# Optimization experiments

Measured on AMD Instinct MI355X. Metric: run time of the kernel, lower is better.

## Reference

```python
import jax, jax.numpy as jnp
import numpy as np

B, H, W = 4, 192, 448
BWEIGHT = 5.0   # backward_weight for level 3
K, P, DC = 5, 2, 25  # unfold/dist kernel, padding, dist channels


def conv(x, w, b, pad):
    y = jax.lax.conv_general_dilated(x, w, (1, 1), pad,
                                     dimension_numbers=('NCHW', 'OIHW', 'NCHW'))
    return y + b[None, :, None, None]


def lrelu(x):
    return jnp.where(x >= 0, x, 0.1 * x)


def backwarp(img, flow):
    # bilinear backward warp, zero padding, align_corners=True convention
    _, C, h, w = img.shape
    yy, xx = jnp.meshgrid(jnp.arange(h, dtype=img.dtype), jnp.arange(w, dtype=img.dtype), indexing='ij')
    x = xx[None] + flow[:, 0]  # [B,H,W] absolute sample coords
    y = yy[None] + flow[:, 1]
    x0 = jnp.floor(x); y0 = jnp.floor(y)
    wx1 = x - x0; wy1 = y - y0
    wx0 = 1.0 - wx1; wy0 = 1.0 - wy1

    def gather(yi, xi):
        valid = ((yi >= 0) & (yi < h) & (xi >= 0) & (xi < w)).astype(img.dtype)
        yc = jnp.clip(yi, 0, h - 1).astype(jnp.int32)
        xc = jnp.clip(xi, 0, w - 1).astype(jnp.int32)
        v = jax.vmap(lambda im, yv, xv: im[:, yv, xv])(img, yc, xc)  # [B,C,H,W]
        return v * valid[:, None]

    return (gather(y0, x0) * (wy0 * wx0)[:, None] + gather(y0, x0 + 1) * (wy0 * wx1)[:, None]
            + gather(y0 + 1, x0) * (wy1 * wx0)[:, None] + gather(y0 + 1, x0 + 1) * (wy1 * wx1)[:, None])


def unfold1(x):
    # x: [B,1,H,W] -> [B,K*K,H,W], patch order (kh,kw) row-major like torch unfold
    return jax.lax.conv_general_dilated_patches(x, (K, K), (1, 1), ((P, P), (P, P)))


def setup_inputs() -> dict:
    key = jax.random.key(0)
    ks = jax.random.split(key, 24)
    f32 = jnp.float32
    inp = {
        'tensor1': jax.random.normal(ks[0], (B, 3, H, W), f32),
        'tensor2': jax.random.normal(ks[1], (B, 3, H, W), f32),
        'features_tensor1': jax.random.normal(ks[2], (B, 64, H, W), f32),
        'features_tensor2': jax.random.normal(ks[3], (B, 64, H, W), f32),
        'flow_tensor': jax.random.normal(ks[4], (B, 2, H, W), f32) * 2.0,
    }

    def wgt(i, shape):
        fan = int(np.prod(shape[1:]))
        return jax.random.normal(ks[i], shape, f32) / np.sqrt(fan)

    inp['feat_w'] = wgt(5, (128, 64, 1, 1)); inp['feat_b'] = jnp.zeros((128,), f32)
    inp['main_w1'] = wgt(6, (128, 131, 3, 3)); inp['main_b1'] = jnp.zeros((128,), f32)
    inp['main_w2'] = wgt(7, (128, 128, 3, 3)); inp['main_b2'] = jnp.zeros((128,), f32)
    inp['main_w3'] = wgt(8, (64, 128, 3, 3)); inp['main_b3'] = jnp.zeros((64,), f32)
    inp['main_w4'] = wgt(9, (64, 64, 3, 3)); inp['main_b4'] = jnp.zeros((64,), f32)
    inp['main_w5'] = wgt(10, (32, 64, 3, 3)); inp['main_b5'] = jnp.zeros((32,), f32)
    inp['main_w6'] = wgt(11, (32, 32, 3, 3)); inp['main_b6'] = jnp.zeros((32,), f32)
    inp['dist_w1'] = wgt(12, (DC, 32, K, 1)); inp['dist_b1'] = jnp.zeros((DC,), f32)
    inp['dist_w2'] = wgt(13, (DC, DC, 1, K)); inp['dist_b2'] = jnp.zeros((DC,), f32)
    inp['sx_w'] = wgt(14, (1, DC, 1, 1)); inp['sx_b'] = jnp.zeros((1,), f32)
    inp['sy_w'] = wgt(15, (1, DC, 1, 1)); inp['sy_b'] = jnp.zeros((1,), f32)
    return inp


def reference(tensor1, tensor2, features_tensor1, features_tensor2, flow_tensor,
              feat_w, feat_b, main_w1, main_b1, main_w2, main_b2, main_w3, main_b3,
              main_w4, main_b4, main_w5, main_b5, main_w6, main_b6,
              dist_w1, dist_b1, dist_w2, dist_b2, sx_w, sx_b, sy_w, sy_b):
    z = ((0, 0), (0, 0))
    o = ((1, 1), (1, 1))
    warp = backwarp(tensor2, flow_tensor * BWEIGHT)
    diff = jax.lax.stop_gradient(jnp.sqrt(jnp.sum((tensor1 - warp) ** 2, axis=1, keepdims=True)))
    feat = lrelu(conv(features_tensor1, feat_w, feat_b, z))
    flow_c = flow_tensor - jnp.mean(flow_tensor, axis=(2, 3), keepdims=True)
    x = jnp.concatenate([diff, flow_c, feat], axis=1)  # [B,131,H,W]
    for w, b in [(main_w1, main_b1), (main_w2, main_b2), (main_w3, main_b3),
                 (main_w4, main_b4), (main_w5, main_b5), (main_w6, main_b6)]:
        x = lrelu(conv(x, w, b, o))
    dist = conv(x, dist_w1, dist_b1, ((P, P), (0, 0)))   # 5x1 conv
    dist = conv(dist, dist_w2, dist_b2, ((0, 0), (P, P)))  # 1x5 conv
    dist = -(dist * dist)
    dist = jnp.exp(dist - jnp.max(dist, axis=1, keepdims=True))  # [B,25,H,W]
    divisor = 1.0 / jnp.sum(dist, axis=1, keepdims=True)
    u1 = unfold1(flow_tensor[:, 0:1])  # [B,25,H,W]
    u2 = unfold1(flow_tensor[:, 1:2])
    sx = conv(dist * u1, sx_w, sx_b, z) * divisor
    sy = conv(dist * u2, sy_w, sy_b, z) * divisor
    return jnp.concatenate([sx, sy], axis=1)
```

## Files before the change

kernel.cpp:

```cpp
#include <hip/hip_runtime.h>
#include <math.h>

#define HH 192
#define WW 448
#define HW (HH * WW)
#define PW2 450
#define PH2 194
#define NPAD 87300
#define NPADT 87552
#define GUARD 1024
#define NB 4

typedef _Float16 half8 __attribute__((ext_vector_type(8)));
typedef _Float16 half4v __attribute__((ext_vector_type(4)));
typedef float float4v __attribute__((ext_vector_type(4)));

__global__ void mean_kernel(const float* __restrict__ flow, float* __restrict__ means) {
    int bc = blockIdx.x;
    const float* src = flow + (size_t)bc * HW;
    float s = 0.f;
    for (int i = threadIdx.x; i < HW; i += 256) s += src[i];
    __shared__ float red[256];
    red[threadIdx.x] = s;
    __syncthreads();
    for (int off = 128; off > 0; off >>= 1) {
        if (threadIdx.x < off) red[threadIdx.x] += red[threadIdx.x + off];
        __syncthreads();
    }
    if (threadIdx.x == 0) means[bc] = red[0] * (1.0f / (float)HW);
}

__global__ void wtrans_kernel(const float* __restrict__ w, _Float16* __restrict__ wt,
                              int cinReal, int nchunk, int cout, int nshift, int perm,
                              int total) {
    int idx = blockIdx.x * 256 + threadIdx.x;
    if (idx >= total) return;
    int k = idx & 31;
    int r = idx >> 5;
    int m = r % cout;
    int r2 = r / cout;
    int q = r2 % nchunk;
    int s = r2 / nchunk;
    int icb = q * 32 + k;
    float val = 0.f;
    if (perm) {
        if (icb < 131) {
            int icr = (icb < 128) ? icb + 3 : icb - 128;
            val = w[((size_t)m * cinReal + icr) * nshift + s];
        }
    } else if (icb < cinReal) {
        val = w[((size_t)m * cinReal + icb) * nshift + s];
    }
    wt[idx] = (_Float16)val;
}

__global__ void feat_transpose(const float* __restrict__ feat, _Float16* __restrict__ F,
                               size_t fSlot) {
    __shared__ _Float16 tile[64 * 72];
    int t = threadIdx.x;
    int z = blockIdx.y;
    int pix0 = blockIdx.x * 64;
    const float* src = feat + (size_t)z * 64 * HW + pix0;
#pragma unroll
    for (int pass = 0; pass < 16; ++pass) {
        int c = pass * 4 + (t >> 6);
        int pl = t & 63;
        tile[pl * 72 + c] = (_Float16)src[(size_t)c * HW + pl];
    }
    __syncthreads();
    int row = pix0 / WW;
    int xcol = pix0 - row * WW;
    size_t n0 = (size_t)(row + 1) * PW2 + xcol + 1;
    _Float16* dst = F + (size_t)z * fSlot + n0 * 64;
#pragma unroll
    for (int pass = 0; pass < 2; ++pass) {
        int pl = (t >> 3) + pass * 32;
        int seg = t & 7;
        *(half8*)&dst[(size_t)pl * 64 + seg * 8] = *(const half8*)&tile[pl * 72 + seg * 8];
    }
}

__global__ void prep_kernel(const float* __restrict__ t1, const float* __restrict__ t2,
                            const float* __restrict__ flow, const float* __restrict__ means,
                            _Float16* __restrict__ bufA, size_t aSlot) {
    int n = blockIdx.x * 256 + threadIdx.x;
    if (n >= NPAD) return;
    int z = blockIdx.y;
    _Float16* dst = bufA + (size_t)z * aSlot + (size_t)n * 160 + 128;
    int y = n / PW2, x = n - PW2 * y;
    if (y < 1 || y > HH || x < 1 || x > WW) {
        dst[0] = (_Float16)0.f; dst[1] = (_Float16)0.f; dst[2] = (_Float16)0.f;
        return;
    }
    int iy = y - 1, ix = x - 1, pix = iy * WW + ix;
    const float* fb = flow + (size_t)z * 2 * HW;
    float fx = fb[pix];
    float fy = fb[HW + pix];
    float sx = (float)ix + fx * 5.0f;
    float sy = (float)iy + fy * 5.0f;
    float fx0 = floorf(sx), fy0 = floorf(sy);
    float wx1 = sx - fx0, wy1 = sy - fy0;
    float wx0 = 1.f - wx1, wy0 = 1.f - wy1;
    int ix0 = (int)fx0, iy0 = (int)fy0;
    bool y0ok = (iy0 >= 0) && (iy0 < HH);
    bool y1ok = (iy0 + 1 >= 0) && (iy0 + 1 < HH);
    bool x0ok = (ix0 >= 0) && (ix0 < WW);
    bool x1ok = (ix0 + 1 >= 0) && (ix0 + 1 < WW);
    float d2 = 0.f;
    for (int c = 0; c < 3; ++c) {
        const float* img = t2 + ((size_t)z * 3 + c) * HW;
        float v00 = (y0ok && x0ok) ? img[iy0 * WW + ix0] : 0.f;
        float v01 = (y0ok && x1ok) ? img[iy0 * WW + ix0 + 1] : 0.f;
        float v10 = (y1ok && x0ok) ? img[(iy0 + 1) * WW + ix0] : 0.f;
        float v11 = (y1ok && x1ok) ? img[(iy0 + 1) * WW + ix0 + 1] : 0.f;
        float v = v00 * (wy0 * wx0) + v01 * (wy0 * wx1) + v10 * (wy1 * wx0) + v11 * (wy1 * wx1);
        float d = t1[((size_t)z * 3 + c) * HW + pix] - v;
        d2 += d * d;
    }
    dst[0] = (_Float16)sqrtf(d2);
    dst[1] = (_Float16)(fx - means[z * 2 + 0]);
    dst[2] = (_Float16)(fy - means[z * 2 + 1]);
}

template <int BM, int KH, int KW, int CSIN, int NCHUNK, int CSOUT>
__launch_bounds__(256, 2)
__global__ void mfma_conv(const _Float16* __restrict__ in, size_t inSlot,
                          const _Float16* __restrict__ wt,
                          const float* __restrict__ bias,
                          _Float16* __restrict__ out, size_t outSlot) {
    constexpr int MT = BM / 32;
    __shared__ __align__(16) _Float16 Alds[BM * 72];
    __shared__ __align__(16) _Float16 Blds[128 * 72];
    const int t = threadIdx.x;
    const int wave = t >> 6, lane = t & 63;
    const int wm = wave >> 1, wn = wave & 1;
    const int col = lane & 15, quad = lane >> 4;
    const int n0 = blockIdx.x * 128;
    const _Float16* inImg = in + (size_t)blockIdx.z * inSlot;
    _Float16* outImg = out + (size_t)blockIdx.z * outSlot;

    float4v acc[MT][4];
#pragma unroll
    for (int i = 0; i < MT; ++i)
#pragma unroll
        for (int j = 0; j < 4; ++j) acc[i][j] = float4v{0.f, 0.f, 0.f, 0.f};

    for (int s = 0; s < KH * KW; ++s) {
        const int off = (s / KW - KH / 2) * PW2 + (s % KW - KW / 2);
        const _Float16* bsrc = inImg + (ptrdiff_t)(n0 + off) * CSIN;
        for (int q = 0; q < NCHUNK; ++q) {
            __syncthreads();
            const _Float16* asrc = wt + ((size_t)(s * NCHUNK + q)) * BM * 32;
            for (int i = t; i < BM * 4; i += 256) {
                int m = i >> 2, kp = (i & 3) * 8;
                *(half8*)&Alds[m * 72 + kp] = *(const half8*)&asrc[m * 32 + kp];
            }
            for (int i = t; i < 512; i += 256) {
                int n = i >> 2, kp = (i & 3) * 8;
                *(half8*)&Blds[n * 72 + kp] =
                    *(const half8*)&bsrc[(ptrdiff_t)n * CSIN + q * 32 + kp];
            }
            __syncthreads();
            half8 a[MT], b[4];
#pragma unroll
            for (int mt = 0; mt < MT; ++mt)
                a[mt] = *(const half8*)&Alds[(wm * MT * 16 + mt * 16 + col) * 72 + quad * 8];
#pragma unroll
            for (int nt = 0; nt < 4; ++nt)
                b[nt] = *(const half8*)&Blds[(wn * 64 + nt * 16 + col) * 72 + quad * 8];
#pragma unroll
            for (int mt = 0; mt < MT; ++mt)
#pragma unroll
                for (int nt = 0; nt < 4; ++nt)
                    acc[mt][nt] = __builtin_amdgcn_mfma_f32_16x16x32_f16(
                        a[mt], b[nt], acc[mt][nt], 0, 0, 0);
        }
    }
#pragma unroll
    for (int mt = 0; mt < MT; ++mt) {
        const int m0 = wm * MT * 16 + mt * 16 + quad * 4;
        float bv[4];
#pragma unroll
        for (int i = 0; i < 4; ++i) bv[i] = bias[m0 + i];
#pragma unroll
        for (int nt = 0; nt < 4; ++nt) {
            int n = n0 + wn * 64 + nt * 16 + col;
            int y = n / PW2, x = n - y * PW2;
            bool ok = (y >= 1) && (y <= HH) && (x >= 1) && (x <= WW) && (n < NPAD);
            half4v h;
#pragma unroll
            for (int i = 0; i < 4; ++i) {
                float v = acc[mt][nt][i] + bv[i];
                v = (v >= 0.f) ? v : 0.1f * v;
                h[i] = ok ? (_Float16)v : (_Float16)0.f;
            }
            *(half4v*)&outImg[(size_t)n * CSOUT + m0] = h;
        }
    }
}

__global__ void dist1_kernel(const _Float16* __restrict__ in, size_t inSlot,
                             const float* __restrict__ w, const float* __restrict__ bias,
                             float* __restrict__ outD, size_t outSlot) {
    __shared__ float wl[25 * 32 * 5];
    int t = threadIdx.x;
    for (int i = t; i < 4000; i += 256) wl[i] = w[i];
    __syncthreads();
    int p = blockIdx.x * 256 + t;
    int z = blockIdx.y;
    const _Float16* inI = in + (size_t)z * inSlot;
    float* out = outD + (size_t)z * outSlot;
    int y = p / WW, x = p - y * WW;
    float acc[25];
#pragma unroll
    for (int oc = 0; oc < 25; ++oc) acc[oc] = bias[oc];
    for (int kh = 0; kh < 5; ++kh) {
        int yy = y + kh - 2;
        if (yy < 0 || yy >= HH) continue;
        const _Float16* src = inI + (size_t)((yy + 1) * PW2 + x + 1) * 32;
        _Float16 vals[32];
#pragma unroll
        for (int g = 0; g < 4; ++g) *(half8*)&vals[g * 8] = *(const half8*)&src[g * 8];
#pragma unroll
        for (int ic = 0; ic < 32; ++ic) {
            float v = (float)vals[ic];
#pragma unroll
            for (int oc = 0; oc < 25; ++oc)
                acc[oc] = fmaf(v, wl[(oc * 32 + ic) * 5 + kh], acc[oc]);
        }
    }
#pragma unroll
    for (int oc = 0; oc < 25; ++oc) out[(size_t)p * 25 + oc] = acc[oc];
}

__global__ void final_kernel(const float* __restrict__ D1, size_t d1Slot,
                             const float* __restrict__ flow,
                             const float* __restrict__ dw2, const float* __restrict__ db2,
                             const float* __restrict__ sxw, const float* __restrict__ sxb,
                             const float* __restrict__ syw, const float* __restrict__ syb,
                             float* __restrict__ out) {
    __shared__ float wl[25 * 25 * 5];
    int t = threadIdx.x;
    for (int i = t; i < 3125; i += 256) wl[i] = dw2[i];
    __syncthreads();
    int p = blockIdx.x * 256 + t;
    int z = blockIdx.y;
    const float* D = D1 + (size_t)z * d1Slot;
    int y = p / WW, x = p - y * WW;
    float acc[25];
#pragma unroll
    for (int oc = 0; oc < 25; ++oc) acc[oc] = db2[oc];
    for (int kw = 0; kw < 5; ++kw) {
        int xx = x + kw - 2;
        if (xx < 0 || xx >= WW) continue;
        const float* src = D + (size_t)(y * WW + xx) * 25;
#pragma unroll
        for (int ic = 0; ic < 25; ++ic) {
            float v = src[ic];
#pragma unroll
            for (int oc = 0; oc < 25; ++oc)
                acc[oc] = fmaf(v, wl[(oc * 25 + ic) * 5 + kw], acc[oc]);
        }
    }
    float e[25];
    float m = -1e30f;
#pragma unroll
    for (int c = 0; c < 25; ++c) {
        float d = -(acc[c] * acc[c]);
        e[c] = d;
        m = fmaxf(m, d);
    }
    float s = 0.f;
#pragma unroll
    for (int c = 0; c < 25; ++c) {
        e[c] = expf(e[c] - m);
        s += e[c];
    }
    const float* f0 = flow + (size_t)z * 2 * HW;
    const float* f1 = f0 + HW;
    float ax = sxb[0], ay = syb[0];
#pragma unroll
    for (int kh = 0; kh < 5; ++kh) {
        int iy = y + kh - 2;
        bool yok = (iy >= 0) && (iy < HH);
#pragma unroll
        for (int kw = 0; kw < 5; ++kw) {
            int ix = x + kw - 2;
            int c = kh * 5 + kw;
            float u1 = 0.f, u2 = 0.f;
            if (yok && ix >= 0 && ix < WW) {
                int q = iy * WW + ix;
                u1 = f0[q];
                u2 = f1[q];
            }
            ax = fmaf(e[c] * u1, sxw[c], ax);
            ay = fmaf(e[c] * u2, syw[c], ay);
        }
    }
    float inv = 1.0f / s;
    out[(size_t)z * 2 * HW + p] = ax * inv;
    out[(size_t)z * 2 * HW + HW + p] = ay * inv;
}

extern "C" void kernel_launch(void* const* d_in, const int* in_sizes, int n_in,
                              void* d_out, int out_size, void* d_ws, size_t ws_size,
                              hipStream_t stream) {
    const float* t1      = (const float*)d_in[0];
    const float* t2      = (const float*)d_in[1];
    const float* feat_in = (const float*)d_in[2];
    const float* flow    = (const float*)d_in[4];
    const float* feat_w  = (const float*)d_in[5];
    const float* feat_b  = (const float*)d_in[6];
    const float* w1 = (const float*)d_in[7];   const float* b1 = (const float*)d_in[8];
    const float* w2 = (const float*)d_in[9];   const float* b2 = (const float*)d_in[10];
    const float* w3 = (const float*)d_in[11];  const float* b3 = (const float*)d_in[12];
    const float* w4 = (const float*)d_in[13];  const float* b4 = (const float*)d_in[14];
    const float* w5 = (const float*)d_in[15];  const float* b5 = (const float*)d_in[16];
    const float* w6 = (const float*)d_in[17];  const float* b6 = (const float*)d_in[18];
    const float* dw1 = (const float*)d_in[19]; const float* db1 = (const float*)d_in[20];
    const float* dw2 = (const float*)d_in[21]; const float* db2 = (const float*)d_in[22];
    const float* sxw = (const float*)d_in[23]; const float* sxb = (const float*)d_in[24];
    const float* syw = (const float*)d_in[25]; const float* syb = (const float*)d_in[26];
    float* out = (float*)d_out;
    char* ws = (char*)d_ws;

    const size_t OFF_FEAT = 0;
    const size_t OFF_C1 = 8192;
    const size_t OFF_C2 = 192512;
    const size_t OFF_C3 = 339968;
    const size_t OFF_C4 = 413696;
    const size_t OFF_C5 = 450560;
    const size_t OFF_C6 = 468992;
    const size_t WT_BYTES = 478208 * 2;

    _Float16* wt = (_Float16*)ws;
    float* means = (float*)(ws + WT_BYTES);
    const size_t F0 = WT_BYTES + 64;
    const size_t F_SLOT_B = (size_t)(NPADT + 2 * GUARD) * 64 * 2;
    const size_t A_SLOT_B = (size_t)(NPADT + 2 * GUARD) * 160 * 2;
    const size_t B_SLOT_B = (size_t)(NPADT + 2 * GUARD) * 128 * 2;
    const size_t C_SLOT_B = B_SLOT_B;
    const size_t PER_IMG = F_SLOT_B + A_SLOT_B + B_SLOT_B + C_SLOT_B;
    const size_t needFull = F0 + NB * PER_IMG;
    const int step = (ws_size >= needFull) ? NB : 1;

    const size_t A0 = F0 + step * F_SLOT_B;
    const size_t B0 = A0 + step * A_SLOT_B;
    const size_t C0 = B0 + step * B_SLOT_B;

    _Float16* Fd    = (_Float16*)(ws + F0) + (size_t)GUARD * 64;
    _Float16* Ad    = (_Float16*)(ws + A0) + (size_t)GUARD * 160;
    _Float16* Bd128 = (_Float16*)(ws + B0) + (size_t)GUARD * 128;
    _Float16* Bd64  = (_Float16*)(ws + B0) + (size_t)GUARD * 64;
    _Float16* Bd32  = (_Float16*)(ws + B0) + (size_t)GUARD * 32;
    _Float16* Cd128 = (_Float16*)(ws + C0) + (size_t)GUARD * 128;
    _Float16* Cd64  = (_Float16*)(ws + C0) + (size_t)GUARD * 64;
    _Float16* Cd32  = (_Float16*)(ws + C0) + (size_t)GUARD * 32;
    float* D1 = (float*)(ws + F0);

    const size_t FSL = F_SLOT_B / 2, ASL = A_SLOT_B / 2, BSL = B_SLOT_B / 2,
                 CSL = C_SLOT_B / 2, DSL = F_SLOT_B / 4;

    mean_kernel<<<8, 256, 0, stream>>>(flow, means);

    auto wlaunch = [&](const float* src, size_t dst, int cin, int nch, int cout,
                       int nsh, int perm) {
        int total = nsh * nch * cout * 32;
        wtrans_kernel<<<(total + 255) / 256, 256, 0, stream>>>(
            src, wt + dst, cin, nch, cout, nsh, perm, total);
    };
    wlaunch(feat_w, OFF_FEAT, 64, 2, 128, 1, 0);
    wlaunch(w1, OFF_C1, 131, 5, 128, 9, 1);
    wlaunch(w2, OFF_C2, 128, 4, 128, 9, 0);
    wlaunch(w3, OFF_C3, 128, 4, 64, 9, 0);
    wlaunch(w4, OFF_C4, 64, 2, 64, 9, 0);
    wlaunch(w5, OFF_C5, 64, 2, 32, 9, 0);
    wlaunch(w6, OFF_C6, 32, 1, 32, 9, 0);

    const int NT = NPADT / 128;

    for (int b0 = 0; b0 < NB; b0 += step) {
        dim3 gconv(NT, 1, step);
        feat_transpose<<<dim3(HW / 64, step), 256, 0, stream>>>(
            feat_in + (size_t)b0 * 64 * HW, Fd, FSL);
        prep_kernel<<<dim3((NPAD + 255) / 256, step), 256, 0, stream>>>(
            t1 + (size_t)b0 * 3 * HW, t2 + (size_t)b0 * 3 * HW,
            flow + (size_t)b0 * 2 * HW, means + b0 * 2, Ad, ASL);
        mfma_conv<128, 1, 1, 64, 2, 160><<<gconv, 256, 0, stream>>>(
            Fd, FSL, wt + OFF_FEAT, feat_b, Ad, ASL);
        mfma_conv<128, 3, 3, 160, 5, 128><<<gconv, 256, 0, stream>>>(
            Ad, ASL, wt + OFF_C1, b1, Bd128, BSL);
        mfma_conv<128, 3, 3, 128, 4, 128><<<gconv, 256, 0, stream>>>(
            Bd128, BSL, wt + OFF_C2, b2, Cd128, CSL);
        mfma_conv<64, 3, 3, 128, 4, 64><<<gconv, 256, 0, stream>>>(
            Cd128, CSL, wt + OFF_C3, b3, Bd64, BSL);
        mfma_conv<64, 3, 3, 64, 2, 64><<<gconv, 256, 0, stream>>>(
            Bd64, BSL, wt + OFF_C4, b4, Cd64, CSL);
        mfma_conv<32, 3, 3, 64, 2, 32><<<gconv, 256, 0, stream>>>(
            Cd64, CSL, wt + OFF_C5, b5, Bd32, BSL);
        mfma_conv<32, 3, 3, 32, 1, 32><<<gconv, 256, 0, stream>>>(
            Bd32, BSL, wt + OFF_C6, b6, Cd32, CSL);
        dist1_kernel<<<dim3(HW / 256, step), 256, 0, stream>>>(
            Cd32, CSL, dw1, db1, D1, DSL);
        final_kernel<<<dim3(HW / 256, step), 256, 0, stream>>>(
            D1, DSL, flow + (size_t)b0 * 2 * HW, dw2, db2, sxw, sxb, syw, syb,
            out + (size_t)b0 * 2 * HW);
    }
}
```

Before: 1.373 ms.

## Load MFMA fragments directly from global memory with register double-buffering

Removes the shared-memory staging of the weight and input tiles in the implicit-GEMM conv. Each lane now loads its MFMA fragments straight from global memory, prefetching the next k-step into a second register buffer while the current one is multiplied. This removes both per-step barriers and the shared-memory footprint, and raises the occupancy hint in launch bounds. In exchange, loads are now redundant across waves (each wave fetches its own A/B pieces, relying on cache), the fully unrolled loop may inflate code size, and there is more register pressure.

```diff
diff --git a/kernel.cpp b/kernel.cpp
--- a/kernel.cpp
+++ b/kernel.cpp
@@ -123,14 +123,13 @@
 }
 
 template <int BM, int KH, int KW, int CSIN, int NCHUNK, int CSOUT>
-__launch_bounds__(256, 2)
+__launch_bounds__(256, (BM > 64) ? 3 : 4)
 __global__ void mfma_conv(const _Float16* __restrict__ in, size_t inSlot,
                           const _Float16* __restrict__ wt,
                           const float* __restrict__ bias,
                           _Float16* __restrict__ out, size_t outSlot) {
     constexpr int MT = BM / 32;
-    __shared__ __align__(16) _Float16 Alds[BM * 72];
-    __shared__ __align__(16) _Float16 Blds[128 * 72];
+    constexpr int NIT = KH * KW * NCHUNK;
     const int t = threadIdx.x;
     const int wave = t >> 6, lane = t & 63;
     const int wm = wave >> 1, wn = wave & 1;
@@ -139,43 +138,42 @@
     const _Float16* inImg = in + (size_t)blockIdx.z * inSlot;
     _Float16* outImg = out + (size_t)blockIdx.z * outSlot;
 
+    const _Float16* aBase = wt + ((size_t)(wm * MT * 16 + col)) * 32 + quad * 8;
+    const _Float16* bBase = inImg + ((ptrdiff_t)(n0 + wn * 64 + col)) * CSIN + quad * 8;
+
     float4v acc[MT][4];
 #pragma unroll
     for (int i = 0; i < MT; ++i)
 #pragma unroll
         for (int j = 0; j < 4; ++j) acc[i][j] = float4v{0.f, 0.f, 0.f, 0.f};
 
-    for (int s = 0; s < KH * KW; ++s) {
+    half8 aF[2][MT], bF[2][4];
+    auto ld = [&](int it, int buf) {
+        const int s = it / NCHUNK, q = it - s * NCHUNK;
         const int off = (s / KW - KH / 2) * PW2 + (s % KW - KW / 2);
-        const _Float16* bsrc = inImg + (ptrdiff_t)(n0 + off) * CSIN;
-        for (int q = 0; q < NCHUNK; ++q) {
-            __syncthreads();
-            const _Float16* asrc = wt + ((size_t)(s * NCHUNK + q)) * BM * 32;
-            for (int i = t; i < BM * 4; i += 256) {
-                int m = i >> 2, kp = (i & 3) * 8;
-                *(half8*)&Alds[m * 72 + kp] = *(const half8*)&asrc[m * 32 + kp];
-            }
-            for (int i = t; i < 512; i += 256) {
-                int n = i >> 2, kp = (i & 3) * 8;
-                *(half8*)&Blds[n * 72 + kp] =
-                    *(const half8*)&bsrc[(ptrdiff_t)n * CSIN + q * 32 + kp];
-            }
-            __syncthreads();
-            half8 a[MT], b[4];
-#pragma unroll
-            for (int mt = 0; mt < MT; ++mt)
-                a[mt] = *(const half8*)&Alds[(wm * MT * 16 + mt * 16 + col) * 72 + quad * 8];
+        const _Float16* ap = aBase + (size_t)it * (BM * 32);
+#pragma unroll
+        for (int mt = 0; mt < MT; ++mt)
+            aF[buf][mt] = *(const half8*)(ap + mt * 16 * 32);
+        const _Float16* bp = bBase + (ptrdiff_t)off * CSIN + q * 32;
+#pragma unroll
+        for (int nt = 0; nt < 4; ++nt)
+            bF[buf][nt] = *(const half8*)(bp + (ptrdiff_t)nt * 16 * CSIN);
+    };
+
+    ld(0, 0);
+#pragma unroll
+    for (int it = 0; it < NIT; ++it) {
+        const int cur = it & 1;
+        if (it + 1 < NIT) ld(it + 1, cur ^ 1);
+#pragma unroll
+        for (int mt = 0; mt < MT; ++mt)
 #pragma unroll
             for (int nt = 0; nt < 4; ++nt)
-                b[nt] = *(const half8*)&Blds[(wn * 64 + nt * 16 + col) * 72 + quad * 8];
-#pragma unroll
-            for (int mt = 0; mt < MT; ++mt)
-#pragma unroll
-                for (int nt = 0; nt < 4; ++nt)
-                    acc[mt][nt] = __builtin_amdgcn_mfma_f32_16x16x32_f16(
-                        a[mt], b[nt], acc[mt][nt], 0, 0, 0);
-        }
-    }
+                acc[mt][nt] = __builtin_amdgcn_mfma_f32_16x16x32_f16(
+                    aF[cur][mt], bF[cur][nt], acc[mt][nt], 0, 0, 0);
+    }
+
 #pragma unroll
     for (int mt = 0; mt < MT; ++mt) {
         const int m0 = wm * MT * 16 + mt * 16 + quad * 4;
```

Result: slower. 1.635 ms (+19.1%).

## Load conv B tiles via direct global-to-LDS DMA and read weights from global

Applied to the files above, without the earlier changes.

The MFMA conv kernel drops the weight tile from shared memory, so each wave loads its A fragments directly from global memory into registers. The input tile is copied with global_load_lds into an unpadded 128x32 LDS buffer instead of going through registers. Occupancy bounds go from 2 to 4 blocks per CU, and the tap and chunk loops are fully unrolled. This cuts LDS footprint and VGPR staging traffic, but the unpadded LDS rows may cause bank conflicts. Weight reads from global now happen per wave rather than being shared through LDS.

```diff
diff --git a/kernel.cpp b/kernel.cpp
--- a/kernel.cpp
+++ b/kernel.cpp
@@ -123,14 +123,13 @@
 }
 
 template <int BM, int KH, int KW, int CSIN, int NCHUNK, int CSOUT>
-__launch_bounds__(256, 2)
+__launch_bounds__(256, 4)
 __global__ void mfma_conv(const _Float16* __restrict__ in, size_t inSlot,
                           const _Float16* __restrict__ wt,
                           const float* __restrict__ bias,
                           _Float16* __restrict__ out, size_t outSlot) {
     constexpr int MT = BM / 32;
-    __shared__ __align__(16) _Float16 Alds[BM * 72];
-    __shared__ __align__(16) _Float16 Blds[128 * 72];
+    __shared__ __align__(16) _Float16 Blds[128 * 32];
     const int t = threadIdx.x;
     const int wave = t >> 6, lane = t & 63;
     const int wm = wave >> 1, wn = wave & 1;
@@ -139,41 +138,47 @@
     const _Float16* inImg = in + (size_t)blockIdx.z * inSlot;
     _Float16* outImg = out + (size_t)blockIdx.z * outSlot;
 
+    const _Float16* dmaBase =
+        inImg + (ptrdiff_t)(n0 + wave * 16 + (lane >> 2)) * CSIN + (lane & 3) * 8;
+    _Float16* dst0 = &Blds[(wave * 16) * 32];
+    _Float16* dst1 = &Blds[(64 + wave * 16) * 32];
+    const _Float16* aBase = wt + ((size_t)(wm * MT * 16 + col)) * 32 + quad * 8;
+
     float4v acc[MT][4];
 #pragma unroll
     for (int i = 0; i < MT; ++i)
 #pragma unroll
         for (int j = 0; j < 4; ++j) acc[i][j] = float4v{0.f, 0.f, 0.f, 0.f};
 
+#pragma unroll
     for (int s = 0; s < KH * KW; ++s) {
         const int off = (s / KW - KH / 2) * PW2 + (s % KW - KW / 2);
-        const _Float16* bsrc = inImg + (ptrdiff_t)(n0 + off) * CSIN;
+        const _Float16* gs = dmaBase + (ptrdiff_t)off * CSIN;
+        const _Float16* as = aBase + (size_t)s * NCHUNK * BM * 32;
+#pragma unroll
         for (int q = 0; q < NCHUNK; ++q) {
             __syncthreads();
-            const _Float16* asrc = wt + ((size_t)(s * NCHUNK + q)) * BM * 32;
-            for (int i = t; i < BM * 4; i += 256) {
-                int m = i >> 2, kp = (i & 3) * 8;
-                *(half8*)&Alds[m * 72 + kp] = *(const half8*)&asrc[m * 32 + kp];
-            }
-            for (int i = t; i < 512; i += 256) {
-                int n = i >> 2, kp = (i & 3) * 8;
-                *(half8*)&Blds[n * 72 + kp] =
-                    *(const half8*)&bsrc[(ptrdiff_t)n * CSIN + q * 32 + kp];
-            }
+            __builtin_amdgcn_global_load_lds(
+                (const __attribute__((address_space(1))) void*)(gs + q * 32),
+                (__attribute__((address_space(3))) void*)dst0, 16, 0, 0);
+            __builtin_amdgcn_global_load_lds(
+                (const __attribute__((address_space(1))) void*)(gs + q * 32 + 64 * CSIN),
+                (__attribute__((address_space(3))) void*)dst1, 16, 0, 0);
+            half8 aF[MT];
+#pragma unroll
+            for (int mt = 0; mt < MT; ++mt)
+                aF[mt] = *(const half8*)(as + (size_t)q * BM * 32 + mt * 16 * 32);
             __syncthreads();
-            half8 a[MT], b[4];
-#pragma unroll
-            for (int mt = 0; mt < MT; ++mt)
-                a[mt] = *(const half8*)&Alds[(wm * MT * 16 + mt * 16 + col) * 72 + quad * 8];
+            half8 bF[4];
 #pragma unroll
             for (int nt = 0; nt < 4; ++nt)
-                b[nt] = *(const half8*)&Blds[(wn * 64 + nt * 16 + col) * 72 + quad * 8];
+                bF[nt] = *(const half8*)&Blds[(wn * 64 + nt * 16 + col) * 32 + quad * 8];
 #pragma unroll
             for (int mt = 0; mt < MT; ++mt)
 #pragma unroll
                 for (int nt = 0; nt < 4; ++nt)
                     acc[mt][nt] = __builtin_amdgcn_mfma_f32_16x16x32_f16(
-                        a[mt], b[nt], acc[mt][nt], 0, 0, 0);
+                        aF[mt], bF[nt], acc[mt][nt], 0, 0, 0);
         }
     }
 #pragma unroll
```

Result: faster. 1.248 ms (-9.1%).
